# Performance work log

Hardware: AMD Instinct MI355X
Metric: run time of the kernel (lower is better)

The kernel has to match this reference:

```python
import jax, jax.numpy as jnp
import numpy as np

EPS = 1e-5
NEG_SLOPE = 0.1
K = 3
KK = K * K
PAD = 1


def conv3x3(x, w, b):
    # x: [B,C,H,W], w: [O,C,3,3], zero padding 1, stride 1
    y = jax.lax.conv_general_dilated(x, w, (1, 1), [(PAD, PAD), (PAD, PAD)],
                                     dimension_numbers=('NCHW', 'OIHW', 'NCHW'))
    return y + b[None, :, None, None]


def deform_conv(x, off_w, off_b, mod_w, mod_b, w):
    # modulated deformable conv v2 (torchvision.ops.deform_conv2d semantics)
    B, C, H, W = x.shape
    offset = conv3x3(x, off_w, off_b)                      # [B,2*KK,H,W]
    mask = 2.0 * jax.nn.sigmoid(conv3x3(x, mod_w, mod_b))  # [B,KK,H,W]
    off = offset.reshape(B, KK, 2, H, W)                   # (dy,dx) per kernel pos

    ky = (jnp.arange(KK) // K).astype(x.dtype)  # kernel row of tap k
    kx = (jnp.arange(KK) % K).astype(x.dtype)   # kernel col of tap k
    hh = jnp.arange(H, dtype=x.dtype)
    ww = jnp.arange(W, dtype=x.dtype)

    # sampling positions: [B,KK,H,W]
    py = hh[None, None, :, None] - PAD + ky[None, :, None, None] + off[:, :, 0]
    px = ww[None, None, None, :] - PAD + kx[None, :, None, None] + off[:, :, 1]

    y0 = jnp.floor(py)
    x0 = jnp.floor(px)
    dy = py - y0
    dx = px - x0

    x_flat = x.reshape(B, C, H * W)

    def gather(yi, xi):
        # zero-padded bilinear corner gather -> [B,C,KK,H,W]
        valid = (yi >= 0) & (yi < H) & (xi >= 0) & (xi < W)
        yc = jnp.clip(yi, 0, H - 1).astype(jnp.int32)
        xc = jnp.clip(xi, 0, W - 1).astype(jnp.int32)
        idx = (yc * W + xc).reshape(B, 1, KK * H * W)
        g = jnp.take_along_axis(x_flat, jnp.broadcast_to(idx, (B, C, KK * H * W)), axis=2)
        return g.reshape(B, C, KK, H, W) * valid[:, None].astype(x.dtype)

    wy = dy[:, None]  # [B,1,KK,H,W]
    wx = dx[:, None]
    samp = (gather(y0, x0) * (1 - wy) * (1 - wx)
            + gather(y0, x0 + 1) * (1 - wy) * wx
            + gather(y0 + 1, x0) * wy * (1 - wx)
            + gather(y0 + 1, x0 + 1) * wy * wx)
    samp = samp * mask[:, None]
    # main conv as contraction over (C, KK)
    return jnp.einsum('bckhw,ock->bohw', samp, w.reshape(w.shape[0], C, KK))


def batch_norm(x, gamma, beta):
    # training-mode BatchNorm2d: stats over (B,H,W), biased variance
    mean = jnp.mean(x, axis=(0, 2, 3), keepdims=True)
    var = jnp.mean(jnp.square(x - mean), axis=(0, 2, 3), keepdims=True)
    xn = (x - mean) * jax.lax.rsqrt(var + EPS)
    return xn * gamma[None, :, None, None] + beta[None, :, None, None]


def leaky_relu(x):
    return jnp.where(x >= 0, x, NEG_SLOPE * x)


def setup_inputs() -> dict:
    key = jax.random.key(0)
    ks = jax.random.split(key, 12)
    B, C, H, W = 4, 96, 128, 128
    s = 1.0 / np.sqrt(C * KK)
    d = {
        'x': jax.random.normal(ks[0], (B, C, H, W), jnp.float32),
        'd1_off_w': jax.random.normal(ks[1], (2 * KK, C, K, K), jnp.float32) * s,
        'd1_off_b': jnp.zeros((2 * KK,), jnp.float32),
        'd1_mod_w': jax.random.normal(ks[2], (KK, C, K, K), jnp.float32) * s,
        'd1_mod_b': jnp.zeros((KK,), jnp.float32),
        'd1_w': jax.random.normal(ks[3], (C, C, K, K), jnp.float32) * s,
        'd2_off_w': jax.random.normal(ks[4], (2 * KK, C, K, K), jnp.float32) * s,
        'd2_off_b': jnp.zeros((2 * KK,), jnp.float32),
        'd2_mod_w': jax.random.normal(ks[5], (KK, C, K, K), jnp.float32) * s,
        'd2_mod_b': jnp.zeros((KK,), jnp.float32),
        'd2_w': jax.random.normal(ks[6], (C, C, K, K), jnp.float32) * s,
        'bn_g': jnp.ones((C,), jnp.float32),
        'bn_b': jnp.zeros((C,), jnp.float32),
    }
    return d


def reference(x, d1_off_w, d1_off_b, d1_mod_w, d1_mod_b, d1_w,
              d2_off_w, d2_off_b, d2_mod_w, d2_mod_b, d2_w, bn_g, bn_b):
    h = deform_conv(x, d1_off_w, d1_off_b, d1_mod_w, d1_mod_b, d1_w)
    h = leaky_relu(batch_norm(h, bn_g, bn_b))
    h = deform_conv(h, d2_off_w, d2_off_b, d2_mod_w, d2_mod_b, d2_w)
    h = batch_norm(h, bn_g, bn_b)  # same shared BN module (shared params)
    return x + h
```

## Files before the change

kernel.cpp:

```cpp
#include <hip/hip_runtime.h>
#include <math.h>

#define NB 4
#define NC 96
#define NH 128
#define NW 128
#define HWSZ (NH * NW)
#define NK 9
#define AUXC 27
#define CKK (NC * NK)
#define WCS_STEP 1280
#define WCS_SHORTS (27 * WCS_STEP)
#define WBS_STEP 4096
#define WBS_SHORTS (27 * WBS_STEP)
#define PIXB (NC * 2)
#define ZOFF ((unsigned int)(NB * HWSZ * PIXB))

typedef __attribute__((ext_vector_type(8))) short bf16x8;
typedef __attribute__((ext_vector_type(4))) float f32x4;

__device__ __forceinline__ unsigned int bf16r(float f) {
    unsigned int u = __float_as_uint(f);
    u += 0x7fffu + ((u >> 16) & 1u);
    return u >> 16;
}
__device__ __forceinline__ float uaf(unsigned int u) { return __uint_as_float(u); }

__device__ __forceinline__ unsigned int cvtpk(float lo, float hi) {
    unsigned int u;
    asm("v_cvt_pk_bf16_f32 %0, %1, %2" : "=v"(u) : "v"(lo), "v"(hi));
    return u;
}

__device__ __forceinline__ void gload_lds16(const void* g, void* l) {
    __builtin_amdgcn_global_load_lds(
        (const __attribute__((address_space(1))) void*)g,
        (__attribute__((address_space(3))) void*)l, 16, 0, 0);
}

__global__ __launch_bounds__(256) void prep_weights_kernel(
    const float* __restrict__ offw, const float* __restrict__ modw,
    const float* __restrict__ w,
    unsigned short* __restrict__ wcs, unsigned short* __restrict__ wbs)
{
    int idx = blockIdx.x * 256 + threadIdx.x;
    if (idx < WCS_SHORTS) {
        int st = idx / WCS_STEP;
        int r  = idx - st * WCS_STEP;
        int oc = r / 40;
        int k2 = r - oc * 40;
        unsigned short v = 0;
        if (k2 < 32) {
            int tap = st / 3;
            int c   = (st - 3 * tap) * 32 + k2;
            if (oc < 18)      v = (unsigned short)bf16r(offw[oc * CKK + c * NK + tap]);
            else if (oc < 27) v = (unsigned short)bf16r(modw[(oc - 18) * CKK + c * NK + tap]);
        }
        wcs[idx] = v;
    }
    int j = idx - WCS_SHORTS;
    if (j >= 0 && j < WBS_SHORTS) {
        int st = j >> 12;
        int r  = j & 4095;
        int oc = r / 40;
        int k2 = r - oc * 40;
        unsigned short v = 0;
        if (oc < NC && k2 < 32) {
            int tap = st / 3;
            int c   = (st - 3 * tap) * 32 + k2;
            v = (unsigned short)bf16r(w[oc * CKK + c * NK + tap]);
        }
        wbs[j] = v;
    }
}

__global__ __launch_bounds__(256) void nhwc_kernel(
    const float* __restrict__ in, unsigned short* __restrict__ o)
{
    __shared__ unsigned short tile[64][98];
    int t = threadIdx.x;
    int blk = blockIdx.x;
    int b  = blk >> 8;
    int p0 = (blk & 255) * 64;

    if (blk == 0 && t < NC) o[(size_t)NB * HWSZ * NC + t] = 0;

    const float* ib = in + (size_t)b * NC * HWSZ + p0;
#pragma unroll
    for (int r = 0; r < 12; ++r) {
        int e = (r * 256 + t) * 2;
        int c = e >> 6, px = e & 63;
        float2 v = *(const float2*)(ib + c * HWSZ + px);
        tile[px][c]     = (unsigned short)bf16r(v.x);
        tile[px + 1][c] = (unsigned short)bf16r(v.y);
    }
    __syncthreads();

    unsigned short* ob = o + ((size_t)b * HWSZ + p0) * NC;
#pragma unroll
    for (int r = 0; r < 12; ++r) {
        int e = (r * 256 + t) * 2;
        int px = e / 96, c = e - px * 96;
        ushort2 u;
        u.x = tile[px][c];
        u.y = tile[px][c + 1];
        *(ushort2*)(ob + e) = u;
    }
}

__global__ __launch_bounds__(256) void nhwcbn_kernel(
    const float* __restrict__ in, const float* __restrict__ sc,
    unsigned short* __restrict__ o)
{
    __shared__ unsigned short tile[64][98];
    int t = threadIdx.x;
    int blk = blockIdx.x;
    int b  = blk >> 8;
    int p0 = (blk & 255) * 64;

    const float* ib = in + (size_t)b * NC * HWSZ + p0;
#pragma unroll
    for (int r = 0; r < 12; ++r) {
        int e = (r * 256 + t) * 2;
        int c = e >> 6, px = e & 63;
        float scale = sc[c], shift = sc[NC + c];
        float2 v = *(const float2*)(ib + c * HWSZ + px);
        float ox = fmaf(scale, v.x, shift); ox = ox >= 0.f ? ox : 0.1f * ox;
        float oy = fmaf(scale, v.y, shift); oy = oy >= 0.f ? oy : 0.1f * oy;
        tile[px][c]     = (unsigned short)bf16r(ox);
        tile[px + 1][c] = (unsigned short)bf16r(oy);
    }
    __syncthreads();

    unsigned short* ob = o + ((size_t)b * HWSZ + p0) * NC;
#pragma unroll
    for (int r = 0; r < 12; ++r) {
        int e = (r * 256 + t) * 2;
        int px = e / 96, c = e - px * 96;
        ushort2 u;
        u.x = tile[px][c];
        u.y = tile[px][c + 1];
        *(ushort2*)(ob + e) = u;
    }
}

__global__ __launch_bounds__(512, 4) void conv27_mfma_kernel(
    const unsigned short* __restrict__ xhwc,
    const unsigned short* __restrict__ wcs,
    const float* __restrict__ offb, const float* __restrict__ modb,
    float* __restrict__ aux)
{
    __shared__ unsigned int sOff[NK][66];
    __shared__ float sRed[4][8][64];
    __shared__ unsigned short wr[2][2][WCS_STEP];

    int t = threadIdx.x;
    int bid = blockIdx.x;
    int work = ((bid & 7) << 7) | (bid >> 3);
    int base = work * 64;
    int b = base >> 14;
    int rem0 = base & (HWSZ - 1);
    int y = rem0 >> 7;
    int x0 = rem0 & (NW - 1);

    const int lane15   = t & 15;
    const int g        = (t >> 4) & 3;
    const int wv       = t >> 6;
    const int nt       = wv & 3;
    const int ks       = wv >> 2;
    const int px_local = (nt << 4) | lane15;
    const int g8       = g << 3;
    const int l64      = t & 63;

    auto stageC = [&](int st0, int st1, int slot) {
        if (st0 >= 0 && t < 160)
            gload_lds16((const char*)wcs + (size_t)st0 * (WCS_STEP * 2) + t * 16,
                        (char*)&wr[0][slot][0] + t * 16);
        if (st1 >= 0 && t >= 256 && t < 416)
            gload_lds16((const char*)wcs + (size_t)st1 * (WCS_STEP * 2) + (t - 256) * 16,
                        (char*)&wr[1][slot][0] + (t - 256) * 16);
    };

    stageC(0, 14, 0);

    for (int e = t; e < 576; e += 512) {
        int px = e & 63, k = e >> 6;
        int ky = k / 3, kx = k - 3 * (k / 3);
        int yy = y + ky - 1, xx = x0 + px + kx - 1;
        bool v = (yy >= 0) && (yy < NH) && (xx >= 0) && (xx < NW);
        sOff[k][px] = v ? (unsigned int)(((b << 14) + yy * NW + xx) * PIXB)
                        : ZOFF;
    }
    __syncthreads();

    const char* pB = (const char*)xhwc;
    auto loadB = [&](int st) -> bf16x8 {
        int tap = st / 3;
        int c2  = ((st - 3 * tap) * 32 + g8) * 2;
        return *(const bf16x8*)(pB + sOff[tap][px_local] + c2);
    };

    f32x4 acc[2];
    acc[0] = (f32x4){0.f, 0.f, 0.f, 0.f};
    acc[1] = (f32x4){0.f, 0.f, 0.f, 0.f};

    const int stbeg = ks ? 14 : 0;
    const int stend = ks ? 27 : 14;

    bf16x8 bfr = loadB(stbeg);

    for (int i = 0; i < 14; ++i) {
        int stc = stbeg + i;
        stageC((i + 1 < 14) ? i + 1 : -1,
               (15 + i < 27) ? 15 + i : -1, (i + 1) & 1);
        bf16x8 bn = (stc + 1 < stend) ? loadB(stc + 1) : bfr;
        if (stc < stend) {
            bf16x8 a0 = *(const bf16x8*)(&wr[ks][i & 1][lane15 * 40 + g8]);
            bf16x8 a1 = *(const bf16x8*)(&wr[ks][i & 1][(16 + lane15) * 40 + g8]);
            acc[0] = __builtin_amdgcn_mfma_f32_16x16x32_bf16(a0, bfr, acc[0], 0, 0, 0);
            acc[1] = __builtin_amdgcn_mfma_f32_16x16x32_bf16(a1, bfr, acc[1], 0, 0, 0);
        }
        __syncthreads();
        bfr = bn;
    }

    if (ks == 1) {
#pragma unroll
        for (int i = 0; i < 2; ++i)
#pragma unroll
            for (int r = 0; r < 4; ++r)
                sRed[nt][i * 4 + r][l64] = acc[i][r];
    }
    __syncthreads();
    if (ks == 0) {
        float* ap = aux + (size_t)b * AUXC * HWSZ + y * NW + x0 + px_local;
#pragma unroll
        for (int i = 0; i < 2; ++i) {
#pragma unroll
            for (int r = 0; r < 4; ++r) {
                int oc = i * 16 + g * 4 + r;
                float v = acc[i][r] + sRed[nt][i * 4 + r][l64];
                if (oc < 18) {
                    ap[oc * HWSZ] = v + offb[oc];
                } else if (oc < AUXC) {
                    float z = v + modb[oc - 18];
                    ap[oc * HWSZ] = 2.f / (1.f + __expf(-z));
                }
            }
        }
    }
}

__global__ __launch_bounds__(512, 4) void deform_mfma_kernel(
    const unsigned short* __restrict__ xhwc,
    const float* __restrict__ aux,
    const unsigned short* __restrict__ wbs,
    float* __restrict__ out)
{
    __shared__ uint4 sA[NK][NW];
    __shared__ uint2 sW[NK][NW];
    __shared__ unsigned short ws[2][WBS_STEP];

    int t = threadIdx.x;
    int bid = blockIdx.x;
    int work = ((bid & 7) << 6) | (bid >> 3);
    int b = work >> 7;
    int y = work & 127;

    const float* auxb = aux + (size_t)b * AUXC * HWSZ;

    for (int e = t; e < NK * NW; e += 512) {
        int px = e & 127;
        int k  = e >> 7;
        int idx = y * NW + px;
        float offy = auxb[(2 * k) * HWSZ + idx];
        float offx = auxb[(2 * k + 1) * HWSZ + idx];
        float m    = auxb[(18 + k) * HWSZ + idx];
        int ky = k / 3, kx = k - 3 * (k / 3);
        float py  = (float)(y - 1 + ky) + offy;
        float pxf = (float)(px - 1 + kx) + offx;
        float y0f = floorf(py), x0f = floorf(pxf);
        float dy = py - y0f, dx = pxf - x0f;
        int iy0 = (int)y0f, ix0 = (int)x0f;
        int iy1 = iy0 + 1,  ix1 = ix0 + 1;

        bool vy0 = (iy0 >= 0) && (iy0 < NH);
        bool vy1 = (iy1 >= 0) && (iy1 < NH);
        bool vx0 = (ix0 >= 0) && (ix0 < NW);
        bool vx1 = (ix1 >= 0) && (ix1 < NW);
        int cy0 = min(max(iy0, 0), NH - 1);
        int cy1 = min(max(iy1, 0), NH - 1);
        int cx0 = min(max(ix0, 0), NW - 1);
        int cx1 = min(max(ix1, 0), NW - 1);

        float g00 = (1.f - dy) * (1.f - dx) * m; if (!(vy0 && vx0)) g00 = 0.f;
        float g01 = (1.f - dy) * dx * m;         if (!(vy0 && vx1)) g01 = 0.f;
        float g10 = dy * (1.f - dx) * m;         if (!(vy1 && vx0)) g10 = 0.f;
        float g11 = dy * dx * m;                 if (!(vy1 && vx1)) g11 = 0.f;

        uint4 ua;
        ua.x = (unsigned int)(cy0 * NW + cx0) * PIXB;
        ua.y = (unsigned int)(cy0 * NW + cx1) * PIXB;
        ua.z = (unsigned int)(cy1 * NW + cx0) * PIXB;
        ua.w = (unsigned int)(cy1 * NW + cx1) * PIXB;
        uint2 uw;
        uw.x = bf16r(g00) | (bf16r(g01) << 16);
        uw.y = bf16r(g10) | (bf16r(g11) << 16);
        sA[k][px] = ua;
        sW[k][px] = uw;
    }

    gload_lds16((const char*)wbs + (size_t)t * 16, (char*)&ws[0][0] + t * 16);
    __syncthreads();

    f32x4 acc[6];
#pragma unroll
    for (int i = 0; i < 6; ++i) acc[i] = (f32x4){0.f, 0.f, 0.f, 0.f};

    const int lane15   = t & 15;
    const int g        = (t >> 4) & 3;
    const int wv       = t >> 6;
    const int px_local = (wv << 4) | lane15;
    const int g8       = g << 3;

    const char* pB = (const char*)(xhwc + (size_t)b * HWSZ * NC);

    uint4 ga = sA[0][px_local];
    uint2 gw = sW[0][px_local];
    bf16x8 v0 = *(const bf16x8*)(pB + ga.x + (g8 << 1));
    bf16x8 v1 = *(const bf16x8*)(pB + ga.y + (g8 << 1));
    bf16x8 v2 = *(const bf16x8*)(pB + ga.z + (g8 << 1));
    bf16x8 v3 = *(const bf16x8*)(pB + ga.w + (g8 << 1));

    int buf = 0;
    for (int st = 0; st < 27; ++st) {
        bool more = (st + 1 < 27);
        uint4 gaN; uint2 gwN;
        bf16x8 n0, n1, n2, n3;
        if (more) {
            gload_lds16((const char*)wbs + (size_t)(st + 1) * (WBS_STEP * 2) + t * 16,
                        (char*)&ws[buf ^ 1][0] + t * 16);
            int kn  = (st + 1) / 3;
            int c2n = ((st + 1 - 3 * kn) * 32 + g8) * 2;
            gaN = sA[kn][px_local];
            gwN = sW[kn][px_local];
            n0 = *(const bf16x8*)(pB + gaN.x + c2n);
            n1 = *(const bf16x8*)(pB + gaN.y + c2n);
            n2 = *(const bf16x8*)(pB + gaN.z + c2n);
            n3 = *(const bf16x8*)(pB + gaN.w + c2n);
        }

        bf16x8 afr[6];
#pragma unroll
        for (int i = 0; i < 6; ++i)
            afr[i] = *(const bf16x8*)(&ws[buf][(i * 16 + lane15) * 40 + g8]);

        float w00 = uaf(gw.x << 16), w01 = uaf(gw.x & 0xffff0000u);
        float w10 = uaf(gw.y << 16), w11 = uaf(gw.y & 0xffff0000u);
        float s[8];
#pragma unroll
        for (int j = 0; j < 8; ++j) {
            float f0 = uaf((unsigned int)(unsigned short)v0[j] << 16);
            float f1 = uaf((unsigned int)(unsigned short)v1[j] << 16);
            float f2 = uaf((unsigned int)(unsigned short)v2[j] << 16);
            float f3 = uaf((unsigned int)(unsigned short)v3[j] << 16);
            float sv = f0 * w00;
            sv = fmaf(f1, w01, sv);
            sv = fmaf(f2, w10, sv);
            sv = fmaf(f3, w11, sv);
            s[j] = sv;
        }
        union { bf16x8 h; unsigned int u[4]; } uu;
#pragma unroll
        for (int jj = 0; jj < 4; ++jj)
            uu.u[jj] = cvtpk(s[2 * jj], s[2 * jj + 1]);
        bf16x8 bfr = uu.h;

#pragma unroll
        for (int i = 0; i < 6; ++i)
            acc[i] = __builtin_amdgcn_mfma_f32_16x16x32_bf16(afr[i], bfr, acc[i], 0, 0, 0);

        if (more) {
            __syncthreads();
            ga = gaN; gw = gwN; v0 = n0; v1 = n1; v2 = n2; v3 = n3;
            buf ^= 1;
        }
    }

    float* ob = out + (size_t)b * NC * HWSZ + y * NW + px_local;
#pragma unroll
    for (int i = 0; i < 6; ++i) {
        int row0 = i * 16 + g * 4;
#pragma unroll
        for (int r = 0; r < 4; ++r)
            ob[(row0 + r) * HWSZ] = acc[i][r];
    }
}

__global__ __launch_bounds__(256) void bnstats_kernel(
    const float* __restrict__ h, float* __restrict__ part)
{
    int bc = blockIdx.x;
    const float4* p = (const float4*)(h + (size_t)bc * HWSZ);
    float s = 0.f, s2 = 0.f;
    for (int i = threadIdx.x; i < HWSZ / 4; i += 256) {
        float4 v = p[i];
        s  += v.x + v.y + v.z + v.w;
        s2 += v.x * v.x + v.y * v.y + v.z * v.z + v.w * v.w;
    }
#pragma unroll
    for (int o = 32; o > 0; o >>= 1) {
        s  += __shfl_down(s, o);
        s2 += __shfl_down(s2, o);
    }
    __shared__ float red[8];
    int wv = threadIdx.x >> 6, ln = threadIdx.x & 63;
    if (ln == 0) { red[wv] = s; red[4 + wv] = s2; }
    __syncthreads();
    if (threadIdx.x == 0) {
        part[bc]            = red[0] + red[1] + red[2] + red[3];
        part[NB * NC + bc]  = red[4] + red[5] + red[6] + red[7];
    }
}

__global__ __launch_bounds__(128) void bnfinalize_kernel(
    const float* __restrict__ part, const float* __restrict__ g,
    const float* __restrict__ bt, float* __restrict__ sc)
{
    int c = threadIdx.x;
    if (c >= NC) return;
    float s = 0.f, s2 = 0.f;
#pragma unroll
    for (int b = 0; b < NB; ++b) {
        s  += part[b * NC + c];
        s2 += part[NB * NC + b * NC + c];
    }
    const float inv_n = 1.f / (float)(NB * HWSZ);
    float mean = s * inv_n;
    float var  = s2 * inv_n - mean * mean;
    float scale = g[c] * rsqrtf(var + 1e-5f);
    sc[c] = scale;
    sc[NC + c] = bt[c] - mean * scale;
}

__global__ __launch_bounds__(256) void final_kernel(
    float* __restrict__ out, const float* __restrict__ x,
    const float* __restrict__ sc)
{
    const int n4 = NB * NC * HWSZ / 4;
    for (int i = blockIdx.x * 256 + threadIdx.x; i < n4; i += gridDim.x * 256) {
        int c = (i >> 12) % NC;
        float scale = sc[c], shift = sc[NC + c];
        float4 v = ((const float4*)out)[i];
        float4 xv = ((const float4*)x)[i];
        float4 o;
        o.x = xv.x + fmaf(scale, v.x, shift);
        o.y = xv.y + fmaf(scale, v.y, shift);
        o.z = xv.z + fmaf(scale, v.z, shift);
        o.w = xv.w + fmaf(scale, v.w, shift);
        ((float4*)out)[i] = o;
    }
}

extern "C" void kernel_launch(void* const* d_in, const int* in_sizes, int n_in,
                              void* d_out, int out_size, void* d_ws, size_t ws_size,
                              hipStream_t stream)
{
    const float* x        = (const float*)d_in[0];
    const float* d1_off_w = (const float*)d_in[1];
    const float* d1_off_b = (const float*)d_in[2];
    const float* d1_mod_w = (const float*)d_in[3];
    const float* d1_mod_b = (const float*)d_in[4];
    const float* d1_w     = (const float*)d_in[5];
    const float* d2_off_w = (const float*)d_in[6];
    const float* d2_off_b = (const float*)d_in[7];
    const float* d2_mod_w = (const float*)d_in[8];
    const float* d2_mod_b = (const float*)d_in[9];
    const float* d2_w     = (const float*)d_in[10];
    const float* bn_g     = (const float*)d_in[11];
    const float* bn_b     = (const float*)d_in[12];
    float* out = (float*)d_out;

    const size_t nImg = (size_t)NB * NC * HWSZ;
    float* h1   = (float*)d_ws;
    float* aux  = h1   + nImg;
    unsigned short* wcs = (unsigned short*)(aux + (size_t)NB * AUXC * HWSZ);
    unsigned short* wbs = wcs + WCS_SHORTS;
    float* sc   = (float*)(wbs + WBS_SHORTS);
    float* part = sc + 2 * NC;
    unsigned short* xhwc = (unsigned short*)(part + 2 * NB * NC);

    const int npix = NB * HWSZ;
    const int prep_blocks = (WCS_SHORTS + WBS_SHORTS + 255) / 256;

    prep_weights_kernel<<<prep_blocks, 256, 0, stream>>>(d1_off_w, d1_mod_w, d1_w, wcs, wbs);
    nhwc_kernel<<<npix / 64, 256, 0, stream>>>(x, xhwc);
    conv27_mfma_kernel<<<npix / 64, 512, 0, stream>>>(xhwc, wcs, d1_off_b, d1_mod_b, aux);
    deform_mfma_kernel<<<NB * NH, 512, 0, stream>>>(xhwc, aux, wbs, h1);
    bnstats_kernel<<<NB * NC, 256, 0, stream>>>(h1, part);
    bnfinalize_kernel<<<1, 128, 0, stream>>>(part, bn_g, bn_b, sc);

    prep_weights_kernel<<<prep_blocks, 256, 0, stream>>>(d2_off_w, d2_mod_w, d2_w, wcs, wbs);
    nhwcbn_kernel<<<npix / 64, 256, 0, stream>>>(h1, sc, xhwc);
    conv27_mfma_kernel<<<npix / 64, 512, 0, stream>>>(xhwc, wcs, d2_off_b, d2_mod_b, aux);
    deform_mfma_kernel<<<NB * NH, 512, 0, stream>>>(xhwc, aux, wbs, out);
    bnstats_kernel<<<NB * NC, 256, 0, stream>>>(out, part);
    bnfinalize_kernel<<<1, 128, 0, stream>>>(part, bn_g, bn_b, sc);
    final_kernel<<<2048, 256, 0, stream>>>(out, x, sc);
}
```

Baseline: 164.4 us.

## Restructure deform MFMA loop per kernel tap with triple-slab weight staging

The main deformable-conv MFMA loop now runs 9 iterations, one per kernel tap, instead of 27 channel-slab steps. Each iteration stages three weight slabs into LDS at once and issues the gathers for all three channel slabs of the tap early. This cuts the number of __syncthreads barriers and gives more memory-level parallelism for the bilinear gathers. In exchange it triples the LDS weight buffer (about 48KB), which may reduce occupancy, and it raises register pressure from the extra in-flight sample vectors under the 512x4 launch bound.

```diff
diff --git a/kernel.cpp b/kernel.cpp
--- a/kernel.cpp
+++ b/kernel.cpp
@@ -251,6 +251,8 @@
     }
 }
 
+struct Smp { bf16x8 v0, v1, v2, v3; };
+
 __global__ __launch_bounds__(512, 4) void deform_mfma_kernel(
     const unsigned short* __restrict__ xhwc,
     const float* __restrict__ aux,
@@ -259,7 +261,7 @@
 {
     __shared__ uint4 sA[NK][NW];
     __shared__ uint2 sW[NK][NW];
-    __shared__ unsigned short ws[2][WBS_STEP];
+    __shared__ unsigned short ws[2][3 * WBS_STEP];
 
     int t = threadIdx.x;
     int bid = blockIdx.x;
@@ -310,7 +312,13 @@
         sW[k][px] = uw;
     }
 
-    gload_lds16((const char*)wbs + (size_t)t * 16, (char*)&ws[0][0] + t * 16);
+    {
+        const char* gp = (const char*)wbs;
+        char* lp = (char*)&ws[0][0];
+        gload_lds16(gp + t * 16,         lp + t * 16);
+        gload_lds16(gp + 8192 + t * 16,  lp + 8192 + t * 16);
+        gload_lds16(gp + 16384 + t * 16, lp + 16384 + t * 16);
+    }
     __syncthreads();
 
     f32x4 acc[6];
@@ -327,43 +335,30 @@
 
     uint4 ga = sA[0][px_local];
     uint2 gw = sW[0][px_local];
-    bf16x8 v0 = *(const bf16x8*)(pB + ga.x + (g8 << 1));
-    bf16x8 v1 = *(const bf16x8*)(pB + ga.y + (g8 << 1));
-    bf16x8 v2 = *(const bf16x8*)(pB + ga.z + (g8 << 1));
-    bf16x8 v3 = *(const bf16x8*)(pB + ga.w + (g8 << 1));
-
-    int buf = 0;
-    for (int st = 0; st < 27; ++st) {
-        bool more = (st + 1 < 27);
-        uint4 gaN; uint2 gwN;
-        bf16x8 n0, n1, n2, n3;
-        if (more) {
-            gload_lds16((const char*)wbs + (size_t)(st + 1) * (WBS_STEP * 2) + t * 16,
-                        (char*)&ws[buf ^ 1][0] + t * 16);
-            int kn  = (st + 1) / 3;
-            int c2n = ((st + 1 - 3 * kn) * 32 + g8) * 2;
-            gaN = sA[kn][px_local];
-            gwN = sW[kn][px_local];
-            n0 = *(const bf16x8*)(pB + gaN.x + c2n);
-            n1 = *(const bf16x8*)(pB + gaN.y + c2n);
-            n2 = *(const bf16x8*)(pB + gaN.z + c2n);
-            n3 = *(const bf16x8*)(pB + gaN.w + c2n);
-        }
-
+    auto loadSmp = [&](const uint4& a, int j) -> Smp {
+        int c2 = (j * 32 + g8) * 2;
+        Smp s;
+        s.v0 = *(const bf16x8*)(pB + a.x + c2);
+        s.v1 = *(const bf16x8*)(pB + a.y + c2);
+        s.v2 = *(const bf16x8*)(pB + a.z + c2);
+        s.v3 = *(const bf16x8*)(pB + a.w + c2);
+        return s;
+    };
+
+    auto compute = [&](const Smp& sm, const uint2& w, int half, int jslab) {
         bf16x8 afr[6];
 #pragma unroll
         for (int i = 0; i < 6; ++i)
-            afr[i] = *(const bf16x8*)(&ws[buf][(i * 16 + lane15) * 40 + g8]);
-
-        float w00 = uaf(gw.x << 16), w01 = uaf(gw.x & 0xffff0000u);
-        float w10 = uaf(gw.y << 16), w11 = uaf(gw.y & 0xffff0000u);
+            afr[i] = *(const bf16x8*)(&ws[half][jslab * WBS_STEP + (i * 16 + lane15) * 40 + g8]);
+        float w00 = uaf(w.x << 16), w01 = uaf(w.x & 0xffff0000u);
+        float w10 = uaf(w.y << 16), w11 = uaf(w.y & 0xffff0000u);
         float s[8];
 #pragma unroll
         for (int j = 0; j < 8; ++j) {
-            float f0 = uaf((unsigned int)(unsigned short)v0[j] << 16);
-            float f1 = uaf((unsigned int)(unsigned short)v1[j] << 16);
-            float f2 = uaf((unsigned int)(unsigned short)v2[j] << 16);
-            float f3 = uaf((unsigned int)(unsigned short)v3[j] << 16);
+            float f0 = uaf((unsigned int)(unsigned short)sm.v0[j] << 16);
+            float f1 = uaf((unsigned int)(unsigned short)sm.v1[j] << 16);
+            float f2 = uaf((unsigned int)(unsigned short)sm.v2[j] << 16);
+            float f3 = uaf((unsigned int)(unsigned short)sm.v3[j] << 16);
             float sv = f0 * w00;
             sv = fmaf(f1, w01, sv);
             sv = fmaf(f2, w10, sv);
@@ -374,16 +369,42 @@
 #pragma unroll
         for (int jj = 0; jj < 4; ++jj)
             uu.u[jj] = cvtpk(s[2 * jj], s[2 * jj + 1]);
-        bf16x8 bfr = uu.h;
-
 #pragma unroll
         for (int i = 0; i < 6; ++i)
-            acc[i] = __builtin_amdgcn_mfma_f32_16x16x32_bf16(afr[i], bfr, acc[i], 0, 0, 0);
+            acc[i] = __builtin_amdgcn_mfma_f32_16x16x32_bf16(afr[i], uu.h, acc[i], 0, 0, 0);
+    };
+
+    Smp s0 = loadSmp(ga, 0);
+
+    for (int ii = 0; ii < 9; ++ii) {
+        int half = ii & 1;
+        bool more = (ii + 1 < 9);
+        if (more) {
+            const char* gp = (const char*)wbs + (size_t)(ii + 1) * (3 * WBS_STEP * 2);
+            char* lp = (char*)&ws[half ^ 1][0];
+            gload_lds16(gp + t * 16,         lp + t * 16);
+            gload_lds16(gp + 8192 + t * 16,  lp + 8192 + t * 16);
+            gload_lds16(gp + 16384 + t * 16, lp + 16384 + t * 16);
+        }
+
+        Smp s1 = loadSmp(ga, 1);
+        Smp s2 = loadSmp(ga, 2);
+
+        compute(s0, gw, half, 0);
+        compute(s1, gw, half, 1);
+
+        uint4 gaN; uint2 gwN; Smp sN;
+        if (more) {
+            gaN = sA[ii + 1][px_local];
+            gwN = sW[ii + 1][px_local];
+            sN = loadSmp(gaN, 0);
+        }
+
+        compute(s2, gw, half, 2);
 
         if (more) {
             __syncthreads();
-            ga = gaN; gw = gwN; v0 = n0; v1 = n1; v2 = n2; v3 = n3;
-            buf ^= 1;
+            ga = gaN; gw = gwN; s0 = sN;
         }
     }
 
```

Result: slower. 172.1 us (+4.7%).

## Fuse BatchNorm statistics into deformable conv epilogue and drop separate stats pass

Applied to the files above, without the earlier changes.

The deformable conv epilogue now computes per-channel partial sums and sums of squares with lane shuffles and LDS, then writes one partial per block. A new per-channel finalize kernel reduces the 512 partials and computes scale and shift. This removes the separate bnstats pass, which re-read the full activation tensor twice per forward. In exchange it adds shuffle and LDS reduction work and 7.5 KB of extra shared memory to the conv kernel, which may affect occupancy.

```diff
diff --git a/kernel.cpp b/kernel.cpp
--- a/kernel.cpp
+++ b/kernel.cpp
@@ -15,6 +15,7 @@
 #define WBS_SHORTS (27 * WBS_STEP)
 #define PIXB (NC * 2)
 #define ZOFF ((unsigned int)(NB * HWSZ * PIXB))
+#define NBLK 512
 
 typedef __attribute__((ext_vector_type(8))) short bf16x8;
 typedef __attribute__((ext_vector_type(4))) float f32x4;
@@ -255,11 +256,14 @@
     const unsigned short* __restrict__ xhwc,
     const float* __restrict__ aux,
     const unsigned short* __restrict__ wbs,
-    float* __restrict__ out)
+    float* __restrict__ out,
+    float* __restrict__ part)
 {
     __shared__ uint4 sA[NK][NW];
     __shared__ uint2 sW[NK][NW];
     __shared__ unsigned short ws[2][WBS_STEP];
+    __shared__ float redS[8][NC];
+    __shared__ float redQ[8][NC];
 
     int t = threadIdx.x;
     int bid = blockIdx.x;
@@ -388,59 +392,76 @@
     }
 
     float* ob = out + (size_t)b * NC * HWSZ + y * NW + px_local;
+    float sm[6][4], sq[6][4];
 #pragma unroll
     for (int i = 0; i < 6; ++i) {
         int row0 = i * 16 + g * 4;
 #pragma unroll
-        for (int r = 0; r < 4; ++r)
-            ob[(row0 + r) * HWSZ] = acc[i][r];
-    }
-}
-
-__global__ __launch_bounds__(256) void bnstats_kernel(
-    const float* __restrict__ h, float* __restrict__ part)
-{
-    int bc = blockIdx.x;
-    const float4* p = (const float4*)(h + (size_t)bc * HWSZ);
-    float s = 0.f, s2 = 0.f;
-    for (int i = threadIdx.x; i < HWSZ / 4; i += 256) {
-        float4 v = p[i];
-        s  += v.x + v.y + v.z + v.w;
-        s2 += v.x * v.x + v.y * v.y + v.z * v.z + v.w * v.w;
-    }
+        for (int r = 0; r < 4; ++r) {
+            float v = acc[i][r];
+            ob[(row0 + r) * HWSZ] = v;
+            sm[i][r] = v;
+            sq[i][r] = v * v;
+        }
+    }
+#pragma unroll
+    for (int m = 1; m < 16; m <<= 1) {
+#pragma unroll
+        for (int i = 0; i < 6; ++i)
+#pragma unroll
+            for (int r = 0; r < 4; ++r) {
+                sm[i][r] += __shfl_xor(sm[i][r], m);
+                sq[i][r] += __shfl_xor(sq[i][r], m);
+            }
+    }
+    if (lane15 == 0) {
+#pragma unroll
+        for (int i = 0; i < 6; ++i)
+#pragma unroll
+            for (int r = 0; r < 4; ++r) {
+                int ch = i * 16 + g * 4 + r;
+                redS[wv][ch] = sm[i][r];
+                redQ[wv][ch] = sq[i][r];
+            }
+    }
+    __syncthreads();
+    if (t < NC) {
+        float a = 0.f, q = 0.f;
+#pragma unroll
+        for (int w = 0; w < 8; ++w) { a += redS[w][t]; q += redQ[w][t]; }
+        part[(size_t)t * NBLK + work]            = a;
+        part[(size_t)(NC + t) * NBLK + work]     = q;
+    }
+}
+
+__global__ __launch_bounds__(256) void bnfinal2_kernel(
+    const float* __restrict__ part, const float* __restrict__ g,
+    const float* __restrict__ bt, float* __restrict__ sc)
+{
+    int c = blockIdx.x;
+    const float* ps = part + (size_t)c * NBLK;
+    const float* pq = part + (size_t)(NC + c) * NBLK;
+    float s = 0.f, q = 0.f;
+    for (int i = threadIdx.x; i < NBLK; i += 256) { s += ps[i]; q += pq[i]; }
 #pragma unroll
     for (int o = 32; o > 0; o >>= 1) {
-        s  += __shfl_down(s, o);
-        s2 += __shfl_down(s2, o);
+        s += __shfl_down(s, o);
+        q += __shfl_down(q, o);
     }
     __shared__ float red[8];
     int wv = threadIdx.x >> 6, ln = threadIdx.x & 63;
-    if (ln == 0) { red[wv] = s; red[4 + wv] = s2; }
+    if (ln == 0) { red[wv] = s; red[4 + wv] = q; }
     __syncthreads();
     if (threadIdx.x == 0) {
-        part[bc]            = red[0] + red[1] + red[2] + red[3];
-        part[NB * NC + bc]  = red[4] + red[5] + red[6] + red[7];
-    }
-}
-
-__global__ __launch_bounds__(128) void bnfinalize_kernel(
-    const float* __restrict__ part, const float* __restrict__ g,
-    const float* __restrict__ bt, float* __restrict__ sc)
-{
-    int c = threadIdx.x;
-    if (c >= NC) return;
-    float s = 0.f, s2 = 0.f;
-#pragma unroll
-    for (int b = 0; b < NB; ++b) {
-        s  += part[b * NC + c];
-        s2 += part[NB * NC + b * NC + c];
-    }
-    const float inv_n = 1.f / (float)(NB * HWSZ);
-    float mean = s * inv_n;
-    float var  = s2 * inv_n - mean * mean;
-    float scale = g[c] * rsqrtf(var + 1e-5f);
-    sc[c] = scale;
-    sc[NC + c] = bt[c] - mean * scale;
+        float ts = red[0] + red[1] + red[2] + red[3];
+        float tq = red[4] + red[5] + red[6] + red[7];
+        const float inv_n = 1.f / (float)(NB * HWSZ);
+        float mean = ts * inv_n;
+        float var  = tq * inv_n - mean * mean;
+        float scale = g[c] * rsqrtf(var + 1e-5f);
+        sc[c] = scale;
+        sc[NC + c] = bt[c] - mean * scale;
+    }
 }
 
 __global__ __launch_bounds__(256) void final_kernel(
@@ -488,7 +509,7 @@
     unsigned short* wbs = wcs + WCS_SHORTS;
     float* sc   = (float*)(wbs + WBS_SHORTS);
     float* part = sc + 2 * NC;
-    unsigned short* xhwc = (unsigned short*)(part + 2 * NB * NC);
+    unsigned short* xhwc = (unsigned short*)(part + 2 * NC * NBLK);
 
     const int npix = NB * HWSZ;
     const int prep_blocks = (WCS_SHORTS + WBS_SHORTS + 255) / 256;
@@ -496,15 +517,13 @@
     prep_weights_kernel<<<prep_blocks, 256, 0, stream>>>(d1_off_w, d1_mod_w, d1_w, wcs, wbs);
     nhwc_kernel<<<npix / 64, 256, 0, stream>>>(x, xhwc);
     conv27_mfma_kernel<<<npix / 64, 512, 0, stream>>>(xhwc, wcs, d1_off_b, d1_mod_b, aux);
-    deform_mfma_kernel<<<NB * NH, 512, 0, stream>>>(xhwc, aux, wbs, h1);
-    bnstats_kernel<<<NB * NC, 256, 0, stream>>>(h1, part);
-    bnfinalize_kernel<<<1, 128, 0, stream>>>(part, bn_g, bn_b, sc);
+    deform_mfma_kernel<<<NB * NH, 512, 0, stream>>>(xhwc, aux, wbs, h1, part);
+    bnfinal2_kernel<<<NC, 256, 0, stream>>>(part, bn_g, bn_b, sc);
 
     prep_weights_kernel<<<prep_blocks, 256, 0, stream>>>(d2_off_w, d2_mod_w, d2_w, wcs, wbs);
     nhwcbn_kernel<<<npix / 64, 256, 0, stream>>>(h1, sc, xhwc);
     conv27_mfma_kernel<<<npix / 64, 512, 0, stream>>>(xhwc, wcs, d2_off_b, d2_mod_b, aux);
-    deform_mfma_kernel<<<NB * NH, 512, 0, stream>>>(xhwc, aux, wbs, out);
-    bnstats_kernel<<<NB * NC, 256, 0, stream>>>(out, part);
-    bnfinalize_kernel<<<1, 128, 0, stream>>>(part, bn_g, bn_b, sc);
+    deform_mfma_kernel<<<NB * NH, 512, 0, stream>>>(xhwc, aux, wbs, out, part);
+    bnfinal2_kernel<<<NC, 256, 0, stream>>>(part, bn_g, bn_b, sc);
     final_kernel<<<2048, 256, 0, stream>>>(out, x, sc);
 }
```

After: 168.1 us. +2.2%, slower.
